# Kernel optimization log

Measured on AMD Instinct MI355X. Metric: run time of the kernel, lower is better.

Reference implementation:

```python
import jax, jax.numpy as jnp
import numpy as np

B, L, T = 8, 4096, 128
D_H, D_G, D_PROJ = 1024, 256, 256


def setup_inputs() -> dict:
    key = jax.random.key(0)
    k1, k2, k3, k4, k5 = jax.random.split(key, 5)
    H = jax.random.normal(k1, (B, L, D_H), dtype=jnp.float32)
    G = jax.random.normal(k2, (B, T, D_G), dtype=jnp.float32)
    mask = jax.random.randint(k3, (B, L), 0, 2) == 1  # True = masked out
    Wk = jax.random.normal(k4, (D_H, D_PROJ), dtype=jnp.float32) * 0.02
    Wq = jax.random.normal(k5, (D_G, D_PROJ), dtype=jnp.float32) * 0.02
    return {"H": H, "G": G, "mask": mask, "Wk": Wk, "Wq": Wq}


def reference(H, G, mask, Wk, Wq):
    scale = D_PROJ ** (-0.5)
    K = jnp.einsum('bld,dp->blp', H, Wk)          # [B, L, d_proj]
    Q = jnp.einsum('btd,dp->btp', G, Wq)          # [B, T, d_proj]
    logits = jnp.einsum('btp,blp->btl', Q, K) * scale  # [B, T, L]
    logits = jnp.where(mask[:, None, :], -jnp.inf, logits)
    alpha = jax.nn.softmax(logits, axis=-1)       # [B, T, L]
    Z = jnp.einsum('btl,bld->btd', alpha, H)      # [B, T, d_h]
    return Z
```

## Files before the change

kernel.cpp:

```cpp
#include <hip/hip_runtime.h>
#include <hip/hip_bf16.h>
#include <math.h>

#define B_  8
#define L_  4096
#define T_  128
#define DH  1024
#define DG  256
#define DP  256
#define BK  64
#define ZCH 8

typedef short bf16x8 __attribute__((ext_vector_type(8)));
typedef float f32x4  __attribute__((ext_vector_type(4)));
typedef unsigned short u16x8 __attribute__((ext_vector_type(8)));

#define AS1(p) ((const __attribute__((address_space(1))) void*)(p))
#define AS3(p) ((__attribute__((address_space(3))) void*)(p))

#define SYNC() do { asm volatile("s_waitcnt lgkmcnt(0)" ::: "memory"); \
                    __builtin_amdgcn_s_barrier(); \
                    __builtin_amdgcn_sched_barrier(0); } while (0)

__device__ __forceinline__ unsigned short f2bf(float f) {
    unsigned u = __float_as_uint(f);
    unsigned r = (u + 0x7FFFu + ((u >> 16) & 1u)) >> 16;
    return (unsigned short)r;
}

__device__ __forceinline__ char* swz(void* base, int row, int colbytes) {
    return (char*)base + (((row << 7) + colbytes) ^ ((row & 7) << 4));
}
__device__ __forceinline__ const char* swzc(const void* base, int row, int colbytes) {
    return (const char*)base + (((row << 7) + colbytes) ^ ((row & 7) << 4));
}

__global__ __launch_bounds__(256) void wct_kernel(const float* __restrict__ Wk,
                                                  const float* __restrict__ Wq,
                                                  unsigned short* __restrict__ Wct) {
    __shared__ __attribute__((aligned(16))) unsigned short As[128 * BK];
    __shared__ __attribute__((aligned(16))) unsigned short Bs[64 * BK];
    const int n0 = blockIdx.x * 64, m0 = blockIdx.y * 128;
    const int tid = threadIdx.x, wave = tid >> 6, lane = tid & 63;
    const int lm = lane & 15, quad = lane >> 4;
    const int wm = wave >> 1, wn = wave & 1;
    const int bc = (tid & 15) * 4, br = tid >> 4;
    f32x4 acc[4][2] = {};

    for (int k0 = 0; k0 < DP; k0 += BK) {
        #pragma unroll
        for (int s = 0; s < 8; ++s) {
            const int row = br + s * 16;
            const float4 v = *(const float4*)(Wk + (size_t)(m0 + row) * DP + k0 + bc);
            ushort4 p; p.x = f2bf(v.x); p.y = f2bf(v.y); p.z = f2bf(v.z); p.w = f2bf(v.w);
            *(ushort4*)(&As[row * BK + bc]) = p;
        }
        #pragma unroll
        for (int s = 0; s < 4; ++s) {
            const int row = br + s * 16;
            const float4 v = *(const float4*)(Wq + (size_t)(n0 + row) * DP + k0 + bc);
            ushort4 p; p.x = f2bf(v.x); p.y = f2bf(v.y); p.z = f2bf(v.z); p.w = f2bf(v.w);
            *(ushort4*)(&Bs[row * BK + bc]) = p;
        }
        __syncthreads();
        #pragma unroll
        for (int ks = 0; ks < 2; ++ks) {
            bf16x8 a[4], bf[2];
            #pragma unroll
            for (int i = 0; i < 4; ++i)
                a[i] = *(const bf16x8*)(&As[(wm * 64 + i * 16 + lm) * BK + ks * 32 + quad * 8]);
            #pragma unroll
            for (int j = 0; j < 2; ++j)
                bf[j] = *(const bf16x8*)(&Bs[(wn * 32 + j * 16 + lm) * BK + ks * 32 + quad * 8]);
            #pragma unroll
            for (int i = 0; i < 4; ++i)
                #pragma unroll
                for (int j = 0; j < 2; ++j)
                    acc[i][j] = __builtin_amdgcn_mfma_f32_16x16x32_bf16(a[i], bf[j], acc[i][j], 0, 0, 0);
        }
        __syncthreads();
    }
    unsigned short* Cb = Wct + (size_t)m0 * DG + n0;
    #pragma unroll
    for (int i = 0; i < 4; ++i)
        #pragma unroll
        for (int j = 0; j < 2; ++j)
            #pragma unroll
            for (int r = 0; r < 4; ++r)
                Cb[(size_t)(wm * 64 + i * 16 + quad * 4 + r) * DG + wn * 32 + j * 16 + lm] =
                    f2bf(acc[i][j][r] * 0.0625f);
}

__global__ __launch_bounds__(256) void qproj_kernel(const float* __restrict__ G,
                                                    const unsigned short* __restrict__ Wct,
                                                    unsigned short* __restrict__ Qk) {
    __shared__ __attribute__((aligned(16))) unsigned short As[128 * BK];
    __shared__ __attribute__((aligned(16))) unsigned short Bs[64 * BK];
    const int n0 = blockIdx.x * 64, m0 = blockIdx.y * 128;
    const int tid = threadIdx.x, wave = tid >> 6, lane = tid & 63;
    const int lm = lane & 15, quad = lane >> 4;
    const int wm = wave >> 1, wn = wave & 1;
    const int bc = (tid & 15) * 4, br = tid >> 4;
    const int ar = lane >> 3, akb = (lane & 7) * 8;
    f32x4 acc[4][2] = {};

    for (int k0 = 0; k0 < DG; k0 += BK) {
        #pragma unroll
        for (int s = 0; s < 8; ++s) {
            const int row = br + s * 16;
            const float4 v = *(const float4*)(G + (size_t)(m0 + row) * DG + k0 + bc);
            ushort4 p; p.x = f2bf(v.x); p.y = f2bf(v.y); p.z = f2bf(v.z); p.w = f2bf(v.w);
            *(ushort4*)(&As[row * BK + bc]) = p;
        }
        #pragma unroll
        for (int s = 0; s < 2; ++s) {
            const int rowb = s * 32 + wave * 8;
            const unsigned short* gp = Wct + (size_t)(n0 + rowb + ar) * DG + k0 + akb;
            __builtin_amdgcn_global_load_lds(AS1(gp), AS3(&Bs[rowb * BK]), 16, 0, 0);
        }
        __syncthreads();
        #pragma unroll
        for (int ks = 0; ks < 2; ++ks) {
            bf16x8 a[4], bf[2];
            #pragma unroll
            for (int i = 0; i < 4; ++i)
                a[i] = *(const bf16x8*)(&As[(wm * 64 + i * 16 + lm) * BK + ks * 32 + quad * 8]);
            #pragma unroll
            for (int j = 0; j < 2; ++j)
                bf[j] = *(const bf16x8*)(&Bs[(wn * 32 + j * 16 + lm) * BK + ks * 32 + quad * 8]);
            #pragma unroll
            for (int i = 0; i < 4; ++i)
                #pragma unroll
                for (int j = 0; j < 2; ++j)
                    acc[i][j] = __builtin_amdgcn_mfma_f32_16x16x32_bf16(a[i], bf[j], acc[i][j], 0, 0, 0);
        }
        __syncthreads();
    }
    unsigned short* Cb = Qk + (size_t)m0 * DH + n0;
    #pragma unroll
    for (int i = 0; i < 4; ++i)
        #pragma unroll
        for (int j = 0; j < 2; ++j)
            #pragma unroll
            for (int r = 0; r < 4; ++r)
                Cb[(size_t)(wm * 64 + i * 16 + quad * 4 + r) * DH + wn * 32 + j * 16 + lm] =
                    f2bf(acc[i][j][r]);
}

__global__ __launch_bounds__(256, 4) void fusedsm_kernel(const unsigned short* __restrict__ Qk,
                                                         const float* __restrict__ H,
                                                         const int* __restrict__ mask,
                                                         unsigned short* __restrict__ alpha,
                                                         float* __restrict__ rowsum,
                                                         unsigned short* __restrict__ H16) {
    __shared__ __attribute__((aligned(16))) unsigned short As[2][64 * BK];
    __shared__ __attribute__((aligned(16))) unsigned short Bs[2][64 * BK];
    __shared__ float rs[64];
    const int blin = blockIdx.x;
    const int b = blin & 7, rem = blin >> 3;
    const int l0 = (rem >> 1) * 64, t0 = (rem & 1) * 64;
    const int tid = threadIdx.x, wave = tid >> 6, lane = tid & 63;
    const unsigned short* Ab = Qk + ((size_t)b * T_ + t0) * DH;
    const float*          Hb = H + ((size_t)b * L_ + l0) * DH;
    unsigned short*     H16b = H16 + ((size_t)b * L_ + l0) * DH;
    const bool doSpill = (t0 == 0);

    const int lm = lane & 15, quad = lane >> 4;
    const int wm = wave >> 1, wn = wave & 1;
    f32x4 acc[2][2] = {};
    const int ar2 = tid >> 3, ag8 = (tid & 7) * 8;
    const int bc = (tid & 15) * 4, br = tid >> 4;

    if (tid < 64) rs[tid] = 0.f;

    u16x8  qa0[2], qa1[2];
    float4 hv0[4], hv1[4];

    auto LOAD = [&](u16x8* qa, float4* hv, int kd) {
        #pragma unroll
        for (int s = 0; s < 2; ++s)
            qa[s] = *(const u16x8*)(Ab + (size_t)(s * 32 + ar2) * DH + kd + ag8);
        #pragma unroll
        for (int s = 0; s < 4; ++s)
            hv[s] = *(const float4*)(Hb + (size_t)(br + s * 16) * DH + kd + bc);
    };
    auto WRITE = [&](int buf, const u16x8* qa, const float4* hv, int kd) {
        #pragma unroll
        for (int s = 0; s < 2; ++s)
            *(u16x8*)swz(&As[buf][0], s * 32 + ar2, ag8 * 2) = qa[s];
        #pragma unroll
        for (int s = 0; s < 4; ++s) {
            const int row = br + s * 16;
            ushort4 pk; pk.x = f2bf(hv[s].x); pk.y = f2bf(hv[s].y);
            pk.z = f2bf(hv[s].z); pk.w = f2bf(hv[s].w);
            *(ushort4*)swz(&Bs[buf][0], row, bc * 2) = pk;
            if (doSpill) *(ushort4*)(H16b + (size_t)row * DH + kd + bc) = pk;
        }
    };
    auto COMPUTE = [&](int buf) {
        #pragma unroll
        for (int ks = 0; ks < 2; ++ks) {
            bf16x8 a[2], bfv[2];
            #pragma unroll
            for (int i = 0; i < 2; ++i)
                a[i] = *(const bf16x8*)swzc(&As[buf][0], wm * 32 + i * 16 + lm, ks * 64 + quad * 16);
            #pragma unroll
            for (int j = 0; j < 2; ++j)
                bfv[j] = *(const bf16x8*)swzc(&Bs[buf][0], wn * 32 + j * 16 + lm, ks * 64 + quad * 16);
            #pragma unroll
            for (int i = 0; i < 2; ++i)
                #pragma unroll
                for (int j = 0; j < 2; ++j)
                    acc[i][j] = __builtin_amdgcn_mfma_f32_16x16x32_bf16(a[i], bfv[j], acc[i][j], 0, 0, 0);
        }
    };

    const int nT = DH / BK;
    LOAD(qa0, hv0, 0);
    LOAD(qa1, hv1, BK);
    WRITE(0, qa0, hv0, 0);
    SYNC();

    for (int tt = 0; tt < nT; tt += 2) {
        if (tt + 2 < nT) LOAD(qa0, hv0, (tt + 2) * BK);
        COMPUTE(0);
        WRITE(1, qa1, hv1, (tt + 1) * BK);
        SYNC();
        if (tt + 3 < nT) LOAD(qa1, hv1, (tt + 3) * BK);
        COMPUTE(1);
        if (tt + 2 < nT) WRITE(0, qa0, hv0, (tt + 2) * BK);
        SYNC();
    }

    const int c0 = l0 + wn * 32 + lm;
    const int mk0 = mask[(size_t)b * L_ + c0];
    const int mk1 = mask[(size_t)b * L_ + c0 + 16];
    unsigned short* Arow = alpha + ((size_t)b * T_ + t0) * L_ + l0 + wn * 32 + lm;
    #pragma unroll
    for (int i = 0; i < 2; ++i) {
        #pragma unroll
        for (int r = 0; r < 4; ++r) {
            const int row = wm * 32 + i * 16 + quad * 4 + r;
            float e0 = mk0 ? 0.f : __expf(acc[i][0][r]);
            float e1 = mk1 ? 0.f : __expf(acc[i][1][r]);
            Arow[(size_t)row * L_]      = f2bf(e0);
            Arow[(size_t)row * L_ + 16] = f2bf(e1);
            float part = e0 + e1;
            part += __shfl_xor(part, 1, 64);
            part += __shfl_xor(part, 2, 64);
            part += __shfl_xor(part, 4, 64);
            part += __shfl_xor(part, 8, 64);
            if (lm == 0) atomicAdd(&rs[row], part);
        }
    }
    __syncthreads();
    if (tid < 64) atomicAdd(&rowsum[(size_t)b * T_ + t0 + tid], rs[tid]);
}

__global__ __launch_bounds__(256, 3) void z_kernel(const unsigned short* __restrict__ alpha,
                                                   const unsigned short* __restrict__ H16,
                                                   float* __restrict__ part) {
    __shared__ __attribute__((aligned(16))) unsigned short As[2][T_ * BK];
    __shared__ __attribute__((aligned(16))) unsigned B32[2][64 * 32];
    const int blin = blockIdx.x;
    const int ch = blin & 7, rem = blin >> 3;
    const int b = rem & 7, d0 = (rem >> 3) * 64;
    const int tid = threadIdx.x, wave = tid >> 6, lane = tid & 63;
    const int Lc = L_ / ZCH;
    const unsigned short* Ab = alpha + (size_t)b * T_ * L_ + ch * Lc;
    const unsigned short* Hb = H16 + ((size_t)b * L_ + ch * Lc) * DH + d0;

    const int lm = lane & 15, quad = lane >> 4;
    const int wm = wave >> 1, wn = wave & 1;
    f32x4 acc[4][2] = {};
    const int a_r = tid >> 3, a_g = (tid & 7) * 8;
    const int dg = tid & 7, lph = tid >> 3;

    u16x8 qa0[4], qa1[4];
    u16x8 hu0[2], hu1[2];

    auto LOAD = [&](u16x8* qa, u16x8* hu, int kd) {
        #pragma unroll
        for (int s = 0; s < 4; ++s)
            qa[s] = *(const u16x8*)(Ab + (size_t)(s * 32 + a_r) * L_ + kd + a_g);
        hu[0] = *(const u16x8*)(Hb + (size_t)(kd + 2 * lph) * DH + dg * 8);
        hu[1] = *(const u16x8*)(Hb + (size_t)(kd + 2 * lph + 1) * DH + dg * 8);
    };
    auto WRITE = [&](int buf, const u16x8* qa, const u16x8* hu) {
        #pragma unroll
        for (int s = 0; s < 4; ++s)
            *(u16x8*)swz(&As[buf][0], s * 32 + a_r, a_g * 2) = qa[s];
        #pragma unroll
        for (int i = 0; i < 8; ++i) {
            const int d   = dg * 8 + i;
            const int rot = ((i + dg) << 2) & 31;
            B32[buf][d * 32 + ((lph + rot) & 31)] = (unsigned)hu[0][i] | ((unsigned)hu[1][i] << 16);
        }
    };
    auto COMPUTE = [&](int buf) {
        #pragma unroll
        for (int ks = 0; ks < 2; ++ks) {
            bf16x8 a[4], bfv[2];
            #pragma unroll
            for (int i = 0; i < 4; ++i)
                a[i] = *(const bf16x8*)swzc(&As[buf][0], wm * 64 + i * 16 + lm, ks * 64 + quad * 16);
            #pragma unroll
            for (int j = 0; j < 2; ++j) {
                const int d   = wn * 32 + j * 16 + lm;
                const int rot = (((d & 7) + ((d >> 3) & 7)) << 2) & 31;
                bfv[j] = *(const bf16x8*)(&B32[buf][d * 32 + ((ks * 16 + quad * 4 + rot) & 31)]);
            }
            #pragma unroll
            for (int i = 0; i < 4; ++i)
                #pragma unroll
                for (int j = 0; j < 2; ++j)
                    acc[i][j] = __builtin_amdgcn_mfma_f32_16x16x32_bf16(a[i], bfv[j], acc[i][j], 0, 0, 0);
        }
    };

    const int nT = Lc / BK;
    LOAD(qa0, hu0, 0);
    LOAD(qa1, hu1, BK);
    WRITE(0, qa0, hu0);
    SYNC();

    for (int tt = 0; tt < nT; tt += 2) {
        if (tt + 2 < nT) LOAD(qa0, hu0, (tt + 2) * BK);
        COMPUTE(0);
        WRITE(1, qa1, hu1);
        SYNC();
        if (tt + 3 < nT) LOAD(qa1, hu1, (tt + 3) * BK);
        COMPUTE(1);
        if (tt + 2 < nT) WRITE(0, qa0, hu0);
        SYNC();
    }

    float* Cb = part + (((size_t)ch * B_ + b) * T_) * DH + d0;
    #pragma unroll
    for (int i = 0; i < 4; ++i)
        #pragma unroll
        for (int j = 0; j < 2; ++j)
            #pragma unroll
            for (int r = 0; r < 4; ++r)
                Cb[(size_t)(wm * 64 + i * 16 + quad * 4 + r) * DH + wn * 32 + j * 16 + lm] = acc[i][j][r];
}

__global__ __launch_bounds__(256) void zreduce_kernel(const float* __restrict__ p,
                                                      const float* __restrict__ rowsum,
                                                      float* __restrict__ Z) {
    const size_t n = (size_t)B_ * T_ * DH;
    const size_t i = ((size_t)blockIdx.x * 256 + threadIdx.x) * 4;
    const int row = (int)(i >> 10);
    const float inv = 1.0f / rowsum[row];
    float4 o = {0.f, 0.f, 0.f, 0.f};
    #pragma unroll
    for (int c = 0; c < ZCH; ++c) {
        const float4 a = *(const float4*)(p + (size_t)c * n + i);
        o.x += a.x; o.y += a.y; o.z += a.z; o.w += a.w;
    }
    o.x *= inv; o.y *= inv; o.z *= inv; o.w *= inv;
    *(float4*)(Z + i) = o;
}

extern "C" void kernel_launch(void* const* d_in, const int* in_sizes, int n_in,
                              void* d_out, int out_size, void* d_ws, size_t ws_size,
                              hipStream_t stream) {
    const float* H    = (const float*)d_in[0];
    const float* G    = (const float*)d_in[1];
    const int*   mask = (const int*)d_in[2];
    const float* Wk   = (const float*)d_in[3];
    const float* Wq   = (const float*)d_in[4];
    float* Z = (float*)d_out;

    char* ws = (char*)d_ws;
    unsigned short* Wct    = (unsigned short*)ws;
    unsigned short* Qk     = (unsigned short*)(ws + ((size_t)1 << 20));
    unsigned short* alpha  = (unsigned short*)(ws + ((size_t)4 << 20));
    float*          rowsum = (float*)(ws + ((size_t)13 << 20));
    unsigned short* H16    = (unsigned short*)(ws + ((size_t)14 << 20));
    float*          zpart  = (float*)(ws + ((size_t)80 << 20));

    hipMemsetAsync(rowsum, 0, (size_t)B_ * T_ * sizeof(float), stream);
    wct_kernel<<<dim3(DG / 64, DH / 128), 256, 0, stream>>>(Wk, Wq, Wct);
    qproj_kernel<<<dim3(DH / 64, (B_ * T_) / 128), 256, 0, stream>>>(G, Wct, Qk);
    fusedsm_kernel<<<1024, 256, 0, stream>>>(Qk, H, mask, alpha, rowsum, H16);
    z_kernel<<<1024, 256, 0, stream>>>(alpha, H16, zpart);
    zreduce_kernel<<<(B_ * T_ * DH / 4) / 256, 256, 0, stream>>>(zpart, rowsum, Z);
}
```

Measured before the change: 284.4 us.

## Pre-convert H to tiled bf16 layout in separate kernel before logits

Adds a standalone kernel that converts H from fp32 to bf16 and stores it in a 64x64 tiled layout. The fused logits/softmax kernel and the Z kernel then read contiguous bf16 tiles instead of fp32 rows or strided row-major bf16. This stops both t-half blocks of the fused kernel from reading the full fp32 H, and it removes the conditional spill writes. The cost is an extra kernel launch and a full pass over H, with fp32 read and bf16 written, before the GEMMs.

```diff
diff --git a/kernel.cpp b/kernel.cpp
--- a/kernel.cpp
+++ b/kernel.cpp
@@ -33,6 +33,32 @@
 }
 __device__ __forceinline__ const char* swzc(const void* base, int row, int colbytes) {
     return (const char*)base + (((row << 7) + colbytes) ^ ((row & 7) << 4));
+}
+
+__global__ __launch_bounds__(256) void hconv_kernel(const float* __restrict__ H,
+                                                    unsigned short* __restrict__ H16) {
+    const int blin = blockIdx.x;
+    const int b = blin & 7, rem = blin >> 3;
+    const int lt = rem >> 1, half = rem & 1;
+    const int wave = threadIdx.x >> 6, lane = threadIdx.x & 63;
+    const int kt_hi = lane >> 4, kkl = (lane & 15) * 4;
+    const size_t tb = ((size_t)b * 64 + lt) * 16;
+    #pragma unroll
+    for (int p = 0; p < 8; ++p) {
+        const int ll = half * 32 + p * 4 + wave;
+        const float* rp = H + ((size_t)b * L_ + lt * 64 + ll) * DH;
+        float4 f[4];
+        #pragma unroll
+        for (int c = 0; c < 4; ++c)
+            f[c] = *(const float4*)(rp + c * 256 + lane * 4);
+        #pragma unroll
+        for (int c = 0; c < 4; ++c) {
+            ushort4 u; u.x = f2bf(f[c].x); u.y = f2bf(f[c].y);
+            u.z = f2bf(f[c].z); u.w = f2bf(f[c].w);
+            const int kt = c * 4 + kt_hi;
+            *(ushort4*)(H16 + ((tb + kt) << 12) + ll * 64 + kkl) = u;
+        }
+    }
 }
 
 __global__ __launch_bounds__(256) void wct_kernel(const float* __restrict__ Wk,
@@ -148,54 +174,45 @@
 }
 
 __global__ __launch_bounds__(256, 4) void fusedsm_kernel(const unsigned short* __restrict__ Qk,
-                                                         const float* __restrict__ H,
+                                                         const unsigned short* __restrict__ H16,
                                                          const int* __restrict__ mask,
                                                          unsigned short* __restrict__ alpha,
-                                                         float* __restrict__ rowsum,
-                                                         unsigned short* __restrict__ H16) {
+                                                         float* __restrict__ rowsum) {
     __shared__ __attribute__((aligned(16))) unsigned short As[2][64 * BK];
     __shared__ __attribute__((aligned(16))) unsigned short Bs[2][64 * BK];
     __shared__ float rs[64];
     const int blin = blockIdx.x;
     const int b = blin & 7, rem = blin >> 3;
-    const int l0 = (rem >> 1) * 64, t0 = (rem & 1) * 64;
+    const int lt = rem >> 1, l0 = lt * 64, t0 = (rem & 1) * 64;
     const int tid = threadIdx.x, wave = tid >> 6, lane = tid & 63;
     const unsigned short* Ab = Qk + ((size_t)b * T_ + t0) * DH;
-    const float*          Hb = H + ((size_t)b * L_ + l0) * DH;
-    unsigned short*     H16b = H16 + ((size_t)b * L_ + l0) * DH;
-    const bool doSpill = (t0 == 0);
+    const unsigned short* Tb = H16 + (((size_t)b * 64 + lt) << 16);
 
     const int lm = lane & 15, quad = lane >> 4;
     const int wm = wave >> 1, wn = wave & 1;
     f32x4 acc[2][2] = {};
     const int ar2 = tid >> 3, ag8 = (tid & 7) * 8;
-    const int bc = (tid & 15) * 4, br = tid >> 4;
+    const int bll = tid >> 2, bkb = (tid & 3) * 32;
 
     if (tid < 64) rs[tid] = 0.f;
 
-    u16x8  qa0[2], qa1[2];
-    float4 hv0[4], hv1[4];
-
-    auto LOAD = [&](u16x8* qa, float4* hv, int kd) {
+    u16x8 qa0[2], qa1[2];
+    u16x8 hb0[2], hb1[2];
+
+    auto LOAD = [&](u16x8* qa, u16x8* hb, int kt) {
         #pragma unroll
         for (int s = 0; s < 2; ++s)
-            qa[s] = *(const u16x8*)(Ab + (size_t)(s * 32 + ar2) * DH + kd + ag8);
-        #pragma unroll
-        for (int s = 0; s < 4; ++s)
-            hv[s] = *(const float4*)(Hb + (size_t)(br + s * 16) * DH + kd + bc);
-    };
-    auto WRITE = [&](int buf, const u16x8* qa, const float4* hv, int kd) {
+            qa[s] = *(const u16x8*)(Ab + (size_t)(s * 32 + ar2) * DH + kt * BK + ag8);
+        const unsigned short* tp = Tb + ((size_t)kt << 12) + tid * 16;
+        hb[0] = *(const u16x8*)(tp);
+        hb[1] = *(const u16x8*)(tp + 8);
+    };
+    auto WRITE = [&](int buf, const u16x8* qa, const u16x8* hb) {
         #pragma unroll
         for (int s = 0; s < 2; ++s)
             *(u16x8*)swz(&As[buf][0], s * 32 + ar2, ag8 * 2) = qa[s];
-        #pragma unroll
-        for (int s = 0; s < 4; ++s) {
-            const int row = br + s * 16;
-            ushort4 pk; pk.x = f2bf(hv[s].x); pk.y = f2bf(hv[s].y);
-            pk.z = f2bf(hv[s].z); pk.w = f2bf(hv[s].w);
-            *(ushort4*)swz(&Bs[buf][0], row, bc * 2) = pk;
-            if (doSpill) *(ushort4*)(H16b + (size_t)row * DH + kd + bc) = pk;
-        }
+        *(u16x8*)swz(&Bs[buf][0], bll, bkb)      = hb[0];
+        *(u16x8*)swz(&Bs[buf][0], bll, bkb + 16) = hb[1];
     };
     auto COMPUTE = [&](int buf) {
         #pragma unroll
@@ -216,19 +233,19 @@
     };
 
     const int nT = DH / BK;
-    LOAD(qa0, hv0, 0);
-    LOAD(qa1, hv1, BK);
-    WRITE(0, qa0, hv0, 0);
+    LOAD(qa0, hb0, 0);
+    LOAD(qa1, hb1, 1);
+    WRITE(0, qa0, hb0);
     SYNC();
 
     for (int tt = 0; tt < nT; tt += 2) {
-        if (tt + 2 < nT) LOAD(qa0, hv0, (tt + 2) * BK);
+        if (tt + 2 < nT) LOAD(qa0, hb0, tt + 2);
         COMPUTE(0);
-        WRITE(1, qa1, hv1, (tt + 1) * BK);
+        WRITE(1, qa1, hb1);
         SYNC();
-        if (tt + 3 < nT) LOAD(qa1, hv1, (tt + 3) * BK);
+        if (tt + 3 < nT) LOAD(qa1, hb1, tt + 3);
         COMPUTE(1);
-        if (tt + 2 < nT) WRITE(0, qa0, hv0, (tt + 2) * BK);
+        if (tt + 2 < nT) WRITE(0, qa0, hb0);
         SYNC();
     }
 
@@ -264,11 +281,10 @@
     __shared__ __attribute__((aligned(16))) unsigned B32[2][64 * 32];
     const int blin = blockIdx.x;
     const int ch = blin & 7, rem = blin >> 3;
-    const int b = rem & 7, d0 = (rem >> 3) * 64;
+    const int b = rem & 7, dt = rem >> 3, d0 = dt * 64;
     const int tid = threadIdx.x, wave = tid >> 6, lane = tid & 63;
     const int Lc = L_ / ZCH;
     const unsigned short* Ab = alpha + (size_t)b * T_ * L_ + ch * Lc;
-    const unsigned short* Hb = H16 + ((size_t)b * L_ + ch * Lc) * DH + d0;
 
     const int lm = lane & 15, quad = lane >> 4;
     const int wm = wave >> 1, wn = wave & 1;
@@ -279,12 +295,14 @@
     u16x8 qa0[4], qa1[4];
     u16x8 hu0[2], hu1[2];
 
-    auto LOAD = [&](u16x8* qa, u16x8* hu, int kd) {
+    auto LOAD = [&](u16x8* qa, u16x8* hu, int t) {
         #pragma unroll
         for (int s = 0; s < 4; ++s)
-            qa[s] = *(const u16x8*)(Ab + (size_t)(s * 32 + a_r) * L_ + kd + a_g);
-        hu[0] = *(const u16x8*)(Hb + (size_t)(kd + 2 * lph) * DH + dg * 8);
-        hu[1] = *(const u16x8*)(Hb + (size_t)(kd + 2 * lph + 1) * DH + dg * 8);
+            qa[s] = *(const u16x8*)(Ab + (size_t)(s * 32 + a_r) * L_ + t * BK + a_g);
+        const int lt = ch * 8 + t;
+        const unsigned short* tp = H16 + ((((size_t)b * 64 + lt) * 16 + dt) << 12);
+        hu[0] = *(const u16x8*)(tp + (2 * lph) * 64 + dg * 8);
+        hu[1] = *(const u16x8*)(tp + (2 * lph + 1) * 64 + dg * 8);
     };
     auto WRITE = [&](int buf, const u16x8* qa, const u16x8* hu) {
         #pragma unroll
@@ -320,16 +338,16 @@
 
     const int nT = Lc / BK;
     LOAD(qa0, hu0, 0);
-    LOAD(qa1, hu1, BK);
+    LOAD(qa1, hu1, 1);
     WRITE(0, qa0, hu0);
     SYNC();
 
     for (int tt = 0; tt < nT; tt += 2) {
-        if (tt + 2 < nT) LOAD(qa0, hu0, (tt + 2) * BK);
+        if (tt + 2 < nT) LOAD(qa0, hu0, tt + 2);
         COMPUTE(0);
         WRITE(1, qa1, hu1);
         SYNC();
-        if (tt + 3 < nT) LOAD(qa1, hu1, (tt + 3) * BK);
+        if (tt + 3 < nT) LOAD(qa1, hu1, tt + 3);
         COMPUTE(1);
         if (tt + 2 < nT) WRITE(0, qa0, hu0);
         SYNC();
@@ -381,9 +399,10 @@
     float*          zpart  = (float*)(ws + ((size_t)80 << 20));
 
     hipMemsetAsync(rowsum, 0, (size_t)B_ * T_ * sizeof(float), stream);
+    hconv_kernel<<<1024, 256, 0, stream>>>(H, H16);
     wct_kernel<<<dim3(DG / 64, DH / 128), 256, 0, stream>>>(Wk, Wq, Wct);
     qproj_kernel<<<dim3(DH / 64, (B_ * T_) / 128), 256, 0, stream>>>(G, Wct, Qk);
-    fusedsm_kernel<<<1024, 256, 0, stream>>>(Qk, H, mask, alpha, rowsum, H16);
+    fusedsm_kernel<<<1024, 256, 0, stream>>>(Qk, H16, mask, alpha, rowsum);
     z_kernel<<<1024, 256, 0, stream>>>(alpha, H16, zpart);
     zreduce_kernel<<<(B_ * T_ * DH / 4) / 256, 256, 0, stream>>>(zpart, rowsum, Z);
 }
```

Result: no change. 289.3 us (+1.7%).
